# Kernel optimization log

Measured on AMD Instinct MI355X. Metric: run time of the kernel, lower is better.

Reference implementation:

```python
import jax, jax.numpy as jnp
import numpy as np

EMBED = 1024
B, S = 4, 2048


def setup_inputs() -> dict:
    key = jax.random.key(0)
    ks = jax.random.split(key, 10)
    scale = 1.0 / np.sqrt(EMBED)
    return {
        "query": jax.random.normal(ks[0], (B, S, EMBED), jnp.float32),
        "key": jax.random.normal(ks[1], (B, S, EMBED), jnp.float32),
        "value": jax.random.normal(ks[2], (B, S, EMBED), jnp.float32),
        "attn_mask": jnp.zeros((B, S, S), jnp.float32),
        "Wq": jax.random.normal(ks[3], (EMBED, EMBED), jnp.float32) * scale,
        "bq": jnp.zeros((EMBED,), jnp.float32),
        "Wk": jax.random.normal(ks[4], (EMBED, EMBED), jnp.float32) * scale,
        "bk": jnp.zeros((EMBED,), jnp.float32),
        "Wv": jax.random.normal(ks[5], (EMBED, EMBED), jnp.float32) * scale,
        "bv": jnp.zeros((EMBED,), jnp.float32),
    }


def reference(query, key, value, attn_mask, Wq, bq, Wk, bk, Wv, bv):
    # Linear projections (torch Linear: x @ W.T + b)
    q = jnp.einsum("bse,fe->bsf", query, Wq) + bq
    k = jnp.einsum("bse,fe->bsf", key, Wk) + bk
    v = jnp.einsum("bse,fe->bsf", value, Wv) + bv
    # Scaled dot-product attention; NOTE: scale is sqrt(embed_size) (full dim),
    # matching the original module exactly (num_heads is unused there).
    inv_scale = 1.0 / jnp.sqrt(jnp.asarray(q.shape[-1], q.dtype))
    qk = jnp.einsum("bqe,bke->bqk", q, k) * inv_scale + attn_mask
    attn = jax.nn.softmax(qk, axis=-1)
    # dropout_p = 0.0 (eval-mode identity)
    return jnp.einsum("bqk,bke->bqe", attn, v)
```

## Files before the change

### kernel.cpp

```cpp
#include <hip/hip_runtime.h>
#include <stdint.h>


typedef __attribute__((ext_vector_type(8))) short s8v;
typedef __attribute__((ext_vector_type(4))) float f32x4;

__device__ __forceinline__ unsigned short f2b(float f) {
  union { float f; unsigned u; } c; c.f = f;
  unsigned r = c.u + 0x7fffu + ((c.u >> 16) & 1u);
  return (unsigned short)(r >> 16);
}
__device__ __forceinline__ float b2f(unsigned short s) {
  union { float f; unsigned u; } c; c.u = ((unsigned)s) << 16; return c.f;
}

__device__ __forceinline__ void gload_lds16(const void* gsrc, void* ldst) {
  __builtin_amdgcn_global_load_lds(
      (__attribute__((address_space(1))) unsigned int*)(uintptr_t)gsrc,
      (__attribute__((address_space(3))) unsigned int*)(unsigned)(uintptr_t)ldst,
      16, 0, 0);
}

template <bool OUT_BF16, int BIAS, bool MASK>
__global__ __launch_bounds__(256, 2) void gemm_nt(
    const unsigned short* __restrict__ A, long strideAb, int lda,
    const unsigned short* __restrict__ B, long strideBb, int ldb,
    void* __restrict__ Cptr, long strideCb, int ldc,
    const float* __restrict__ bias,
    const float* __restrict__ maskp, long strideMb, int ldM,
    int M, int N, int K, float scale, int tilesN) {
  __shared__ __align__(16) short AsS[128 * 64];
  __shared__ __align__(16) short BsS[128 * 64];

  const int tid = threadIdx.x;
  const int lane = tid & 63;
  const int w = tid >> 6;
  const int wr = w >> 1, wc = w & 1;
  const int batch = blockIdx.y;
  const int tm = blockIdx.x / tilesN, tn = blockIdx.x % tilesN;
  const int brow = tm * 128, bcol = tn * 128;

  const unsigned short* aSrc = A + (long)batch * strideAb +
      (long)(brow + w * 32 + (lane >> 3)) * lda + (lane & 7) * 8;
  const unsigned short* bSrc = B + (long)batch * strideBb +
      (long)(bcol + w * 32 + (lane >> 3)) * ldb + (lane & 7) * 8;

  f32x4 acc[4][4];
#pragma unroll
  for (int i = 0; i < 4; i++)
#pragma unroll
    for (int j = 0; j < 4; j++) acc[i][j] = (f32x4){0.f, 0.f, 0.f, 0.f};

  const int fr = lane & 15;
  const int fq = lane >> 4;
  const int nk = K >> 6;

  for (int kt = 0; kt < nk; kt++) {
#pragma unroll
    for (int i = 0; i < 4; i++) {
      gload_lds16(aSrc + (long)i * 8 * lda, &AsS[w * 2048 + i * 512]);
      gload_lds16(bSrc + (long)i * 8 * ldb, &BsS[w * 2048 + i * 512]);
    }
    aSrc += 64; bSrc += 64;
    __syncthreads();
#pragma unroll
    for (int ks = 0; ks < 2; ks++) {
      s8v af[4], bf[4];
#pragma unroll
      for (int mi = 0; mi < 4; mi++)
        af[mi] = *(const s8v*)&AsS[(wr * 64 + mi * 16 + fr) * 64 + ks * 32 + fq * 8];
#pragma unroll
      for (int ni = 0; ni < 4; ni++)
        bf[ni] = *(const s8v*)&BsS[(wc * 64 + ni * 16 + fr) * 64 + ks * 32 + fq * 8];
#pragma unroll
      for (int mi = 0; mi < 4; mi++)
#pragma unroll
        for (int ni = 0; ni < 4; ni++)
          acc[mi][ni] = __builtin_amdgcn_mfma_f32_16x16x32_bf16(
              af[mi], bf[ni], acc[mi][ni], 0, 0, 0);
    }
    __syncthreads();
  }

  unsigned short* Cb = (unsigned short*)Cptr;
  float* Cf = (float*)Cptr;
  const long cB = (long)batch * strideCb;
  const float* maskB = MASK ? (maskp + (long)batch * strideMb) : nullptr;
#pragma unroll
  for (int mi = 0; mi < 4; mi++) {
#pragma unroll
    for (int ni = 0; ni < 4; ni++) {
      const int col = bcol + wc * 64 + ni * 16 + fr;
#pragma unroll
      for (int r = 0; r < 4; r++) {
        const int row = brow + wr * 64 + mi * 16 + fq * 4 + r;
        float v = acc[mi][ni][r] * scale;
        if (BIAS == 1) v += bias[col];
        if (BIAS == 2) v += bias[row];
        if (MASK) v += maskB[(long)row * ldM + col];
        if (OUT_BF16) Cb[cB + (long)row * ldc + col] = f2b(v);
        else          Cf[cB + (long)row * ldc + col] = v;
      }
    }
  }
}

__global__ __launch_bounds__(256) void cvt_f32_bf16(
    const float* __restrict__ in, unsigned short* __restrict__ out, long n8) {
  long i = (long)blockIdx.x * blockDim.x + threadIdx.x;
  const long stride = (long)gridDim.x * blockDim.x;
  for (; i < n8; i += stride) {
    const float* p = in + i * 8;
    f32x4 a = *(const f32x4*)p;
    f32x4 b = *(const f32x4*)(p + 4);
    s8v o;
    o[0] = (short)f2b(a[0]); o[1] = (short)f2b(a[1]);
    o[2] = (short)f2b(a[2]); o[3] = (short)f2b(a[3]);
    o[4] = (short)f2b(b[0]); o[5] = (short)f2b(b[1]);
    o[6] = (short)f2b(b[2]); o[7] = (short)f2b(b[3]);
    *(s8v*)(out + i * 8) = o;
  }
}

__global__ __launch_bounds__(256) void softmax_inplace(unsigned short* __restrict__ S) {
  const long row = blockIdx.x;
  unsigned short* rp = S + row * 2048;
  const int tid = threadIdx.x, lane = tid & 63, wid = tid >> 6;

  s8v vb = *(const s8v*)&rp[tid * 8];
  float x[8];
#pragma unroll
  for (int j = 0; j < 8; j++) x[j] = b2f((unsigned short)vb[j]);

  float m = x[0];
#pragma unroll
  for (int j = 1; j < 8; j++) m = fmaxf(m, x[j]);
#pragma unroll
  for (int off = 32; off > 0; off >>= 1) m = fmaxf(m, __shfl_xor(m, off, 64));

  __shared__ float red[4];
  if (lane == 0) red[wid] = m;
  __syncthreads();
  m = fmaxf(fmaxf(red[0], red[1]), fmaxf(red[2], red[3]));
  __syncthreads();

  float s = 0.f;
#pragma unroll
  for (int j = 0; j < 8; j++) { x[j] = __expf(x[j] - m); s += x[j]; }
#pragma unroll
  for (int off = 32; off > 0; off >>= 1) s += __shfl_xor(s, off, 64);
  if (lane == 0) red[wid] = s;
  __syncthreads();
  s = red[0] + red[1] + red[2] + red[3];
  const float inv = 1.0f / s;

  s8v ob;
#pragma unroll
  for (int j = 0; j < 8; j++) ob[j] = (short)f2b(x[j] * inv);
  *(s8v*)&rp[tid * 8] = ob;
}

extern "C" void kernel_launch(void* const* d_in, const int* in_sizes, int n_in,
                              void* d_out, int out_size, void* d_ws, size_t ws_size,
                              hipStream_t stream) {
  const float* q    = (const float*)d_in[0];
  const float* k    = (const float*)d_in[1];
  const float* v    = (const float*)d_in[2];
  const float* mask = (const float*)d_in[3];
  const float* Wq   = (const float*)d_in[4];
  const float* bq   = (const float*)d_in[5];
  const float* Wk   = (const float*)d_in[6];
  const float* bk   = (const float*)d_in[7];
  const float* Wv   = (const float*)d_in[8];
  const float* bv   = (const float*)d_in[9];
  float* out = (float*)d_out;

  const size_t MB = 1ull << 20;
  if (ws_size < 134 * MB) return;
  char* ws = (char*)d_ws;
  unsigned short* qb  = (unsigned short*)(ws + 0 * MB);
  unsigned short* kb  = (unsigned short*)(ws + 16 * MB);
  unsigned short* vT  = (unsigned short*)(ws + 32 * MB);
  unsigned short* Sb  = (unsigned short*)(ws + 48 * MB);
  unsigned short* xq  = (unsigned short*)(ws + 80 * MB);
  unsigned short* xk  = (unsigned short*)(ws + 96 * MB);
  unsigned short* xv  = (unsigned short*)(ws + 112 * MB);
  unsigned short* Wqb = (unsigned short*)(ws + 128 * MB);
  unsigned short* Wkb = (unsigned short*)(ws + 130 * MB);
  unsigned short* Wvb = (unsigned short*)(ws + 132 * MB);

  const long NX = 4L * 2048 * 1024;
  const long NW = 1024L * 1024;

  cvt_f32_bf16<<<2048, 256, 0, stream>>>(q, xq, NX / 8);
  cvt_f32_bf16<<<2048, 256, 0, stream>>>(k, xk, NX / 8);
  cvt_f32_bf16<<<2048, 256, 0, stream>>>(v, xv, NX / 8);
  cvt_f32_bf16<<<512, 256, 0, stream>>>(Wq, Wqb, NW / 8);
  cvt_f32_bf16<<<512, 256, 0, stream>>>(Wk, Wkb, NW / 8);
  cvt_f32_bf16<<<512, 256, 0, stream>>>(Wv, Wvb, NW / 8);

  gemm_nt<true, 1, false><<<dim3(64 * 8, 1), 256, 0, stream>>>(
      xq, 0, 1024, Wqb, 0, 1024, (void*)qb, 0, 1024,
      bq, nullptr, 0, 0, 8192, 1024, 1024, 1.0f, 8);
  gemm_nt<true, 1, false><<<dim3(64 * 8, 1), 256, 0, stream>>>(
      xk, 0, 1024, Wkb, 0, 1024, (void*)kb, 0, 1024,
      bk, nullptr, 0, 0, 8192, 1024, 1024, 1.0f, 8);
  gemm_nt<true, 2, false><<<dim3(8 * 16, 4), 256, 0, stream>>>(
      Wvb, 0, 1024, xv, 2048L * 1024, 1024, (void*)vT, 1024L * 2048, 2048,
      bv, nullptr, 0, 0, 1024, 2048, 1024, 1.0f, 16);
  gemm_nt<true, 0, true><<<dim3(16 * 16, 4), 256, 0, stream>>>(
      qb, 2048L * 1024, 1024, kb, 2048L * 1024, 1024, (void*)Sb, 2048L * 2048, 2048,
      nullptr, mask, 2048L * 2048, 2048, 2048, 2048, 1024, 0.03125f, 16);
  softmax_inplace<<<8192, 256, 0, stream>>>(Sb);
  gemm_nt<false, 0, false><<<dim3(16 * 8, 4), 256, 0, stream>>>(
      Sb, 2048L * 2048, 2048, vT, 1024L * 2048, 2048, (void*)out, 2048L * 1024, 1024,
      nullptr, nullptr, 0, 0, 2048, 1024, 2048, 1.0f, 8);
}
```

Before: 261.5 us.

## Rewrite GEMM with larger tiles, 4-slot LDS pipeline, swizzle and XCD remap

The bf16 NT GEMM kernel moves from 128x128 tiles with 256 threads and a single LDS buffer to 256xBN tiles (BN 128 or 256) with 512 threads and a 4-slot LDS ring. Loads run two k-steps ahead using raw vmcnt waits and one barrier per iteration. It also adds an XOR swizzle on LDS addresses to avoid bank conflicts, s_setprio around the MFMA blocks, and a block-index remap that spreads consecutive tiles across the 8 XCDs. The goal is to hide global-load latency and raise data reuse per tile, at the cost of far more LDS and registers, which may limit occupancy to one workgroup per CU.

```diff
diff --git a/kernel.cpp b/kernel.cpp
--- a/kernel.cpp
+++ b/kernel.cpp
@@ -21,65 +21,126 @@
       16, 0, 0);
 }
 
-template <bool OUT_BF16, int BIAS, bool MASK>
-__global__ __launch_bounds__(256, 2) void gemm_nt(
+template <int N> __device__ __forceinline__ void waitvm() {
+  if constexpr (N == 4)      asm volatile("s_waitcnt vmcnt(4)" ::: "memory");
+  else if constexpr (N == 3) asm volatile("s_waitcnt vmcnt(3)" ::: "memory");
+  else                       asm volatile("s_waitcnt vmcnt(0)" ::: "memory");
+}
+
+__device__ __forceinline__ int swz(int o) { return o ^ (((o >> 7) & 7) << 4); }
+
+template <int NFRAG, bool OUT_BF16, int BIAS, bool MASK>
+__global__ __launch_bounds__(512, 2) void gemm_nt(
     const unsigned short* __restrict__ A, long strideAb, int lda,
     const unsigned short* __restrict__ B, long strideBb, int ldb,
     void* __restrict__ Cptr, long strideCb, int ldc,
     const float* __restrict__ bias,
     const float* __restrict__ maskp, long strideMb, int ldM,
-    int M, int N, int K, float scale, int tilesN) {
-  __shared__ __align__(16) short AsS[128 * 64];
-  __shared__ __align__(16) short BsS[128 * 64];
+    int K, float scale, int tilesN, int tilesMN) {
+  constexpr int BN = NFRAG * 64;
+  constexpr int ASLOT = 256 * 64;
+  constexpr int BSLOT = BN * 64;
+  constexpr int SLOT = ASLOT + BSLOT;
+  constexpr int CH = SLOT / 1024;
+  constexpr int GPW = CH / 8;
+  static_assert(4 * SLOT <= 160 * 1024, "LDS budget");
+  __shared__ __align__(16) char lds[4 * SLOT];
+
+  const int nwg = gridDim.x;
+  int bid = blockIdx.x;
+  bid = (bid & 7) * (nwg >> 3) + (bid >> 3);
+  const int batch = bid / tilesMN;
+  const int tt = bid - batch * tilesMN;
+  const int tm = tt / tilesN, tn = tt - tm * tilesN;
+  const int brow = tm << 8, bcol = tn * BN;
 
   const int tid = threadIdx.x;
-  const int lane = tid & 63;
-  const int w = tid >> 6;
-  const int wr = w >> 1, wc = w & 1;
-  const int batch = blockIdx.y;
-  const int tm = blockIdx.x / tilesN, tn = blockIdx.x % tilesN;
-  const int brow = tm * 128, bcol = tn * 128;
-
-  const unsigned short* aSrc = A + (long)batch * strideAb +
-      (long)(brow + w * 32 + (lane >> 3)) * lda + (lane & 7) * 8;
-  const unsigned short* bSrc = B + (long)batch * strideBb +
-      (long)(bcol + w * 32 + (lane >> 3)) * ldb + (lane & 7) * 8;
-
-  f32x4 acc[4][4];
-#pragma unroll
-  for (int i = 0; i < 4; i++)
-#pragma unroll
-    for (int j = 0; j < 4; j++) acc[i][j] = (f32x4){0.f, 0.f, 0.f, 0.f};
-
-  const int fr = lane & 15;
-  const int fq = lane >> 4;
-  const int nk = K >> 6;
-
-  for (int kt = 0; kt < nk; kt++) {
-#pragma unroll
-    for (int i = 0; i < 4; i++) {
-      gload_lds16(aSrc + (long)i * 8 * lda, &AsS[w * 2048 + i * 512]);
-      gload_lds16(bSrc + (long)i * 8 * ldb, &BsS[w * 2048 + i * 512]);
+  const int lane = tid & 63, w = tid >> 6;
+  const int wm = w >> 2, wn = w & 3;
+  const int fr = lane & 15, fq = lane >> 4;
+
+  const unsigned short* gsrc[GPW];
+  int ldsdst[GPW];
+  {
+    const unsigned short* Ab = A + (long)batch * strideAb;
+    const unsigned short* Bb = B + (long)batch * strideBb;
+#pragma unroll
+    for (int i = 0; i < GPW; i++) {
+      const int c = w + i * 8;
+      const bool isA = (c < 16);
+      const int cc = isA ? c : c - 16;
+      const int roff = cc * 1024 + lane * 16;
+      const int logical = swz(roff);
+      const int row = logical >> 6, colb = logical & 63;
+      gsrc[i] = (isA ? (Ab + (long)(brow + row) * lda)
+                     : (Bb + (long)(bcol + row) * ldb)) + (colb >> 1);
+      ldsdst[i] = (isA ? 0 : ASLOT) + cc * 1024;
     }
-    aSrc += 64; bSrc += 64;
-    __syncthreads();
-#pragma unroll
-    for (int ks = 0; ks < 2; ks++) {
-      s8v af[4], bf[4];
-#pragma unroll
-      for (int mi = 0; mi < 4; mi++)
-        af[mi] = *(const s8v*)&AsS[(wr * 64 + mi * 16 + fr) * 64 + ks * 32 + fq * 8];
-#pragma unroll
-      for (int ni = 0; ni < 4; ni++)
-        bf[ni] = *(const s8v*)&BsS[(wc * 64 + ni * 16 + fr) * 64 + ks * 32 + fq * 8];
-#pragma unroll
-      for (int mi = 0; mi < 4; mi++)
-#pragma unroll
-        for (int ni = 0; ni < 4; ni++)
-          acc[mi][ni] = __builtin_amdgcn_mfma_f32_16x16x32_bf16(
-              af[mi], bf[ni], acc[mi][ni], 0, 0, 0);
+  }
+
+  int offA[8], offB[NFRAG];
+#pragma unroll
+  for (int mi = 0; mi < 8; mi++)
+    offA[mi] = swz((wm * 128 + mi * 16 + fr) * 64 + fq * 16);
+#pragma unroll
+  for (int ni = 0; ni < NFRAG; ni++)
+    offB[ni] = ASLOT + swz((wn * (NFRAG * 16) + ni * 16 + fr) * 64 + fq * 16);
+
+  f32x4 acc[8][NFRAG];
+#pragma unroll
+  for (int mi = 0; mi < 8; mi++)
+#pragma unroll
+    for (int ni = 0; ni < NFRAG; ni++) acc[mi][ni] = (f32x4){0.f, 0.f, 0.f, 0.f};
+
+  const int NT = K >> 5;
+
+  auto STAGE = [&](int kt) {
+    char* const sb = lds + (kt & 3) * SLOT;
+#pragma unroll
+    for (int i = 0; i < GPW; i++)
+      gload_lds16(gsrc[i] + (long)kt * 32, sb + ldsdst[i]);
+  };
+
+  STAGE(0);
+  STAGE(1);
+  waitvm<GPW>();
+  __builtin_amdgcn_s_barrier();
+  __builtin_amdgcn_sched_barrier(0);
+
+  for (int t = 0; t < NT; ++t) {
+    const char* sb = lds + (t & 3) * SLOT;
+    if (t + 2 < NT) STAGE(t + 2);
+
+    s8v bf[NFRAG], af[4];
+#pragma unroll
+    for (int ni = 0; ni < NFRAG; ni++) bf[ni] = *(const s8v*)(sb + offB[ni]);
+#pragma unroll
+    for (int mi = 0; mi < 4; mi++) af[mi] = *(const s8v*)(sb + offA[mi]);
+    __builtin_amdgcn_s_setprio(1);
+#pragma unroll
+    for (int mi = 0; mi < 4; mi++)
+#pragma unroll
+      for (int ni = 0; ni < NFRAG; ni++)
+        acc[mi][ni] = __builtin_amdgcn_mfma_f32_16x16x32_bf16(
+            af[mi], bf[ni], acc[mi][ni], 0, 0, 0);
+    __builtin_amdgcn_s_setprio(0);
+#pragma unroll
+    for (int mi = 0; mi < 4; mi++) af[mi] = *(const s8v*)(sb + offA[4 + mi]);
+    __builtin_amdgcn_s_setprio(1);
+#pragma unroll
+    for (int mi = 0; mi < 4; mi++)
+#pragma unroll
+      for (int ni = 0; ni < NFRAG; ni++)
+        acc[4 + mi][ni] = __builtin_amdgcn_mfma_f32_16x16x32_bf16(
+            af[mi], bf[ni], acc[4 + mi][ni], 0, 0, 0);
+    __builtin_amdgcn_s_setprio(0);
+
+    if (t + 1 < NT) {
+      if (t + 2 < NT) waitvm<GPW>();
+      else            waitvm<0>();
+      __builtin_amdgcn_s_barrier();
+      __builtin_amdgcn_sched_barrier(0);
     }
-    __syncthreads();
   }
 
   unsigned short* Cb = (unsigned short*)Cptr;
@@ -87,13 +148,13 @@
   const long cB = (long)batch * strideCb;
   const float* maskB = MASK ? (maskp + (long)batch * strideMb) : nullptr;
 #pragma unroll
-  for (int mi = 0; mi < 4; mi++) {
-#pragma unroll
-    for (int ni = 0; ni < 4; ni++) {
-      const int col = bcol + wc * 64 + ni * 16 + fr;
+  for (int mi = 0; mi < 8; mi++) {
+#pragma unroll
+    for (int ni = 0; ni < NFRAG; ni++) {
+      const int col = bcol + wn * (NFRAG * 16) + ni * 16 + fr;
 #pragma unroll
       for (int r = 0; r < 4; r++) {
-        const int row = brow + wr * 64 + mi * 16 + fq * 4 + r;
+        const int row = brow + wm * 128 + mi * 16 + fq * 4 + r;
         float v = acc[mi][ni][r] * scale;
         if (BIAS == 1) v += bias[col];
         if (BIAS == 2) v += bias[row];
@@ -199,20 +260,20 @@
   cvt_f32_bf16<<<512, 256, 0, stream>>>(Wk, Wkb, NW / 8);
   cvt_f32_bf16<<<512, 256, 0, stream>>>(Wv, Wvb, NW / 8);
 
-  gemm_nt<true, 1, false><<<dim3(64 * 8, 1), 256, 0, stream>>>(
+  gemm_nt<2, true, 1, false><<<dim3(256), 512, 0, stream>>>(
       xq, 0, 1024, Wqb, 0, 1024, (void*)qb, 0, 1024,
-      bq, nullptr, 0, 0, 8192, 1024, 1024, 1.0f, 8);
-  gemm_nt<true, 1, false><<<dim3(64 * 8, 1), 256, 0, stream>>>(
+      bq, nullptr, 0, 0, 1024, 1.0f, 8, 256);
+  gemm_nt<2, true, 1, false><<<dim3(256), 512, 0, stream>>>(
       xk, 0, 1024, Wkb, 0, 1024, (void*)kb, 0, 1024,
-      bk, nullptr, 0, 0, 8192, 1024, 1024, 1.0f, 8);
-  gemm_nt<true, 2, false><<<dim3(8 * 16, 4), 256, 0, stream>>>(
+      bk, nullptr, 0, 0, 1024, 1.0f, 8, 256);
+  gemm_nt<2, true, 2, false><<<dim3(256), 512, 0, stream>>>(
       Wvb, 0, 1024, xv, 2048L * 1024, 1024, (void*)vT, 1024L * 2048, 2048,
-      bv, nullptr, 0, 0, 1024, 2048, 1024, 1.0f, 16);
-  gemm_nt<true, 0, true><<<dim3(16 * 16, 4), 256, 0, stream>>>(
+      bv, nullptr, 0, 0, 1024, 1.0f, 16, 64);
+  gemm_nt<4, true, 0, true><<<dim3(256), 512, 0, stream>>>(
       qb, 2048L * 1024, 1024, kb, 2048L * 1024, 1024, (void*)Sb, 2048L * 2048, 2048,
-      nullptr, mask, 2048L * 2048, 2048, 2048, 2048, 1024, 0.03125f, 16);
+      nullptr, mask, 2048L * 2048, 2048, 1024, 0.03125f, 8, 64);
   softmax_inplace<<<8192, 256, 0, stream>>>(Sb);
-  gemm_nt<false, 0, false><<<dim3(16 * 8, 4), 256, 0, stream>>>(
+  gemm_nt<2, false, 0, false><<<dim3(256), 512, 0, stream>>>(
       Sb, 2048L * 2048, 2048, vT, 1024L * 2048, 2048, (void*)out, 2048L * 1024, 1024,
-      nullptr, nullptr, 0, 0, 2048, 1024, 2048, 1.0f, 8);
-}
+      nullptr, nullptr, 0, 0, 2048, 1.0f, 8, 64);
+}
```

New measurement: 232.7 us. -11.0%, faster.
